# Kernel tuning notes

Hardware: AMD Instinct MI355X
Metric: run time of the kernel (lower is better)

Reference implementation:

```python
import jax, jax.numpy as jnp
import numpy as np

IN_OCT = 512
OUT_OCT = 512
BATCH = 512


def setup_inputs() -> dict:
    key = jax.random.key(0)
    kx, kw = jax.random.split(key)
    x = jax.random.normal(kx, (BATCH, IN_OCT * 8), dtype=jnp.float32)
    weight = jax.random.normal(kw, (OUT_OCT, IN_OCT, 8, 8), dtype=jnp.float32)
    bias = jnp.zeros((OUT_OCT, 8), dtype=jnp.float32)
    return {"x": x, "weight": weight, "bias": bias}


def reference(x, weight, bias):
    # x: [B, in_oct*8]; weight: [out_oct, in_oct, 8, 8]; bias: [out_oct, 8]
    B = x.shape[0]
    out_oct, in_oct = weight.shape[0], weight.shape[1]
    xo = x.reshape(B, in_oct, 8)
    # octonion_mul(x[:, j], weight[i, j]) applies the per-pair 8x8 octonion
    # left-multiplication matrix; summed over j it is one bilinear contraction.
    y = jnp.einsum("bjp,ijpk->bik", xo, weight) + bias[None, :, :]
    return y.reshape(B, out_oct * 8)
```

## Files before the change

kernel.cpp:

```cpp
#include <hip/hip_runtime.h>
#include <stdint.h>


#define M_DIM 512
#define N_DIM 4096
#define K_DIM 4096
#define KSPLIT 8
#define NIT ((K_DIM / KSPLIT) / 32)
#define PART_ELEMS (M_DIM * N_DIM)

typedef __bf16 bf16x8 __attribute__((ext_vector_type(8)));
typedef float f32x4 __attribute__((ext_vector_type(4)));

__device__ inline unsigned short f2bf(float f) {
  union { float f; unsigned int u; } v;
  v.f = f;
  unsigned int u = v.u;
  unsigned int r = (u + 0x7fffu + ((u >> 16) & 1u)) >> 16;
  return (unsigned short)r;
}

__global__ __launch_bounds__(256) void prep_kernel(
    const float* __restrict__ x, const float* __restrict__ w,
    const float* __restrict__ bias, unsigned short* __restrict__ abf,
    unsigned short* __restrict__ bt, float* __restrict__ out) {
  const int bid = blockIdx.x;
  const int t = threadIdx.x;
  if (bid < 4096) {
    __shared__ __align__(16) unsigned short lT[8][512];
    const int i = bid >> 3;
    const int jg = bid & 7;
    const float4* src =
        (const float4*)(w + (size_t)i * 32768 + jg * 4096 + t * 16);
    float4 v0 = src[0], v1 = src[1], v2 = src[2], v3 = src[3];
    const int jp = (t >> 2) * 8 + (t & 3) * 2;
    const float* lo = (const float*)&v0;
    const float* hi = (const float*)&v2;
#pragma unroll
    for (int k = 0; k < 4; ++k) {
      unsigned int pk =
          (unsigned int)f2bf(lo[k]) | ((unsigned int)f2bf(hi[k]) << 16);
      *(unsigned int*)&lT[k][jp] = pk;
    }
    lo = (const float*)&v1;
    hi = (const float*)&v3;
#pragma unroll
    for (int k = 0; k < 4; ++k) {
      unsigned int pk =
          (unsigned int)f2bf(lo[k]) | ((unsigned int)f2bf(hi[k]) << 16);
      *(unsigned int*)&lT[k + 4][jp] = pk;
    }
    __syncthreads();
    const int r = t >> 5, c = t & 31;
    const uint4* s = (const uint4*)&lT[r][c * 16];
    uint4* d = (uint4*)(bt + (size_t)(i * 8 + r) * K_DIM + jg * 512 + c * 16);
    d[0] = s[0];
    d[1] = s[1];
  } else if (bid < 5120) {
    int g = (bid - 4096) * 256 + t;
    const float4* xi = (const float4*)x;
    float4 a = xi[g * 2];
    float4 b = xi[g * 2 + 1];
    __attribute__((aligned(16))) unsigned short o[8] = {
        f2bf(a.x), f2bf(a.y), f2bf(a.z), f2bf(a.w),
        f2bf(b.x), f2bf(b.y), f2bf(b.z), f2bf(b.w)};
    *(uint4*)(abf + (size_t)g * 8) = *(const uint4*)o;
  } else {
    int g = (bid - 5120) * 256 + t;
    int el = g * 4;
    int col = el & (N_DIM - 1);
    *(float4*)(out + el) = *(const float4*)(bias + col);
  }
}

__device__ inline void gld16(const void* g, void* l) {
  __builtin_amdgcn_global_load_lds(
      (const __attribute__((address_space(1))) unsigned int*)g,
      (__attribute__((address_space(3))) unsigned int*)l, 16, 0, 0);
}

__global__ __launch_bounds__(512, 4) void gemm_kernel(
    const unsigned short* __restrict__ A, const unsigned short* __restrict__ Bt,
    float* __restrict__ out, float* __restrict__ part, int use_atomic) {
  __shared__ __align__(16) char lds[2][24 * 1024];
  const int t = threadIdx.x;
  const int n0 = blockIdx.x * 256;
  const int m0 = blockIdx.y * 128;
  const int z = blockIdx.z;
  const int kc0 = z * (K_DIM / KSPLIT);
  const int w = t >> 6;
  const int lane = t & 63;
  const int wr = w >> 2;
  const int wc = w & 3;
  const int lrow = lane & 15;
  const int kb = lane >> 4;

  f32x4 acc[4][4] = {};

  const size_t aOff = (size_t)(m0 + (t >> 2)) * K_DIM + kc0 + (t & 3) * 8;
  const size_t bOff0 = (size_t)(n0 + (t >> 2)) * K_DIM + kc0 + (t & 3) * 8;
  const size_t bOff1 = bOff0 + (size_t)128 * K_DIM;

  auto issue = [&](int it) {
    char* buf = lds[it & 1];
    gld16(A + aOff + it * 32, buf + t * 16);
    gld16(Bt + bOff0 + it * 32, buf + 8192 + t * 16);
    gld16(Bt + bOff1 + it * 32, buf + 16384 + t * 16);
  };

  issue(0);
  for (int it = 0; it < NIT; ++it) {
    __syncthreads();
    if (it + 1 < NIT) issue(it + 1);
    const unsigned short* cA = (const unsigned short*)lds[it & 1];
    const unsigned short* cB = cA + 4096;

    bf16x8 af[4], bfr[4];
#pragma unroll
    for (int mt = 0; mt < 4; ++mt)
      af[mt] = *(const bf16x8*)(cA + (wr * 64 + mt * 16 + lrow) * 32 + kb * 8);
#pragma unroll
    for (int nt = 0; nt < 4; ++nt)
      bfr[nt] = *(const bf16x8*)(cB + (wc * 64 + nt * 16 + lrow) * 32 + kb * 8);
#pragma unroll
    for (int mt = 0; mt < 4; ++mt)
#pragma unroll
      for (int nt = 0; nt < 4; ++nt)
        acc[mt][nt] = __builtin_amdgcn_mfma_f32_16x16x32_bf16(
            af[mt], bfr[nt], acc[mt][nt], 0, 0, 0);
  }

#pragma unroll
  for (int mt = 0; mt < 4; ++mt) {
    const int gmb = m0 + wr * 64 + mt * 16 + kb * 4;
#pragma unroll
    for (int nt = 0; nt < 4; ++nt) {
      const int gn = n0 + wc * 64 + nt * 16 + lrow;
      if (use_atomic) {
#pragma unroll
        for (int r = 0; r < 4; ++r)
          atomicAdd(out + (size_t)(gmb + r) * N_DIM + gn, acc[mt][nt][r]);
      } else {
        float* p = part + (size_t)z * PART_ELEMS;
#pragma unroll
        for (int r = 0; r < 4; ++r)
          p[(size_t)(gmb + r) * N_DIM + gn] = acc[mt][nt][r];
      }
    }
  }
}

__global__ __launch_bounds__(256) void reduce_kernel(
    const float* __restrict__ part, const float* __restrict__ bias,
    float* __restrict__ out) {
  const int g = blockIdx.x * 256 + threadIdx.x;
  const float4* p = (const float4*)part;
  const int Q = PART_ELEMS / 4;
  float4 r = ((const float4*)bias)[g & (N_DIM / 4 - 1)];
#pragma unroll
  for (int z = 0; z < KSPLIT; ++z) {
    float4 s = p[(size_t)g + (size_t)z * Q];
    r.x += s.x;
    r.y += s.y;
    r.z += s.z;
    r.w += s.w;
  }
  ((float4*)out)[g] = r;
}

extern "C" void kernel_launch(void* const* d_in, const int* in_sizes, int n_in,
                              void* d_out, int out_size, void* d_ws,
                              size_t ws_size, hipStream_t stream) {
  const float* x = (const float*)d_in[0];
  const float* w = (const float*)d_in[1];
  const float* bias = (const float*)d_in[2];
  float* out = (float*)d_out;

  unsigned short* abf = (unsigned short*)d_ws;
  unsigned short* bt = abf + (size_t)M_DIM * K_DIM;
  float* part = (float*)((char*)d_ws + 36u * 1024 * 1024);

  const bool have_ws = ws_size >= 101ull * 1024 * 1024;
  const int use_atomic = have_ws ? 0 : 1;

  prep_kernel<<<use_atomic ? 7168 : 5120, 256, 0, stream>>>(x, w, bias, abf,
                                                            bt, out);

  dim3 grid(N_DIM / 256, M_DIM / 128, KSPLIT);
  gemm_kernel<<<grid, 512, 0, stream>>>(abf, bt, out, part, use_atomic);

  if (!use_atomic)
    reduce_kernel<<<PART_ELEMS / 4 / 256, 256, 0, stream>>>(part, bias, out);
}
```

Before: 149.1 us.

## Fuse weight bf16 conversion and transpose into GEMM tile loading

Drops the separate weight conversion pass, which wrote a transposed bf16 copy of the 64 MB fp32 weight. The GEMM now reads fp32 weights directly, converts them in registers and writes them to LDS, prefetching one iteration ahead. Tiles become 512x64 with KSPLIT reduced to 4, which also shrinks the partial-sum buffer and the workspace requirement. The risk is uncoalesced strided fp32 weight loads, with only half the threads loading W, and lower occupancy from the larger LDS footprint.

```diff
diff --git a/kernel.cpp b/kernel.cpp
--- a/kernel.cpp
+++ b/kernel.cpp
@@ -5,8 +5,9 @@
 #define M_DIM 512
 #define N_DIM 4096
 #define K_DIM 4096
-#define KSPLIT 8
-#define NIT ((K_DIM / KSPLIT) / 32)
+#define KSPLIT 4
+#define KC (K_DIM / KSPLIT)
+#define NIT (KC / 32)
 #define PART_ELEMS (M_DIM * N_DIM)
 
 typedef __bf16 bf16x8 __attribute__((ext_vector_type(8)));
@@ -21,43 +22,12 @@
 }
 
 __global__ __launch_bounds__(256) void prep_kernel(
-    const float* __restrict__ x, const float* __restrict__ w,
-    const float* __restrict__ bias, unsigned short* __restrict__ abf,
-    unsigned short* __restrict__ bt, float* __restrict__ out) {
+    const float* __restrict__ x, const float* __restrict__ bias,
+    unsigned short* __restrict__ abf, float* __restrict__ out) {
   const int bid = blockIdx.x;
   const int t = threadIdx.x;
-  if (bid < 4096) {
-    __shared__ __align__(16) unsigned short lT[8][512];
-    const int i = bid >> 3;
-    const int jg = bid & 7;
-    const float4* src =
-        (const float4*)(w + (size_t)i * 32768 + jg * 4096 + t * 16);
-    float4 v0 = src[0], v1 = src[1], v2 = src[2], v3 = src[3];
-    const int jp = (t >> 2) * 8 + (t & 3) * 2;
-    const float* lo = (const float*)&v0;
-    const float* hi = (const float*)&v2;
-#pragma unroll
-    for (int k = 0; k < 4; ++k) {
-      unsigned int pk =
-          (unsigned int)f2bf(lo[k]) | ((unsigned int)f2bf(hi[k]) << 16);
-      *(unsigned int*)&lT[k][jp] = pk;
-    }
-    lo = (const float*)&v1;
-    hi = (const float*)&v3;
-#pragma unroll
-    for (int k = 0; k < 4; ++k) {
-      unsigned int pk =
-          (unsigned int)f2bf(lo[k]) | ((unsigned int)f2bf(hi[k]) << 16);
-      *(unsigned int*)&lT[k + 4][jp] = pk;
-    }
-    __syncthreads();
-    const int r = t >> 5, c = t & 31;
-    const uint4* s = (const uint4*)&lT[r][c * 16];
-    uint4* d = (uint4*)(bt + (size_t)(i * 8 + r) * K_DIM + jg * 512 + c * 16);
-    d[0] = s[0];
-    d[1] = s[1];
-  } else if (bid < 5120) {
-    int g = (bid - 4096) * 256 + t;
+  if (bid < 1024) {
+    int g = bid * 256 + t;
     const float4* xi = (const float4*)x;
     float4 a = xi[g * 2];
     float4 b = xi[g * 2 + 1];
@@ -66,7 +36,7 @@
         f2bf(b.x), f2bf(b.y), f2bf(b.z), f2bf(b.w)};
     *(uint4*)(abf + (size_t)g * 8) = *(const uint4*)o;
   } else {
-    int g = (bid - 5120) * 256 + t;
+    int g = (bid - 1024) * 256 + t;
     int el = g * 4;
     int col = el & (N_DIM - 1);
     *(float4*)(out + el) = *(const float4*)(bias + col);
@@ -79,63 +49,92 @@
       (__attribute__((address_space(3))) unsigned int*)l, 16, 0, 0);
 }
 
-__global__ __launch_bounds__(512, 4) void gemm_kernel(
-    const unsigned short* __restrict__ A, const unsigned short* __restrict__ Bt,
+__global__ __launch_bounds__(512, 2) void gemm_kernel(
+    const unsigned short* __restrict__ A, const float* __restrict__ W,
     float* __restrict__ out, float* __restrict__ part, int use_atomic) {
-  __shared__ __align__(16) char lds[2][24 * 1024];
+  __shared__ __align__(16) char lds[2][36 * 1024];
   const int t = threadIdx.x;
-  const int n0 = blockIdx.x * 256;
-  const int m0 = blockIdx.y * 128;
+  const int bn = blockIdx.x;
+  const int n0 = bn * 64;
   const int z = blockIdx.z;
-  const int kc0 = z * (K_DIM / KSPLIT);
+  const int kc0 = z * KC;
   const int w = t >> 6;
   const int lane = t & 63;
-  const int wr = w >> 2;
-  const int wc = w & 3;
   const int lrow = lane & 15;
   const int kb = lane >> 4;
 
   f32x4 acc[4][4] = {};
 
-  const size_t aOff = (size_t)(m0 + (t >> 2)) * K_DIM + kc0 + (t & 3) * 8;
-  const size_t bOff0 = (size_t)(n0 + (t >> 2)) * K_DIM + kc0 + (t & 3) * 8;
-  const size_t bOff1 = bOff0 + (size_t)128 * K_DIM;
-
-  auto issue = [&](int it) {
+  auto issueA = [&](int it) {
     char* buf = lds[it & 1];
-    gld16(A + aOff + it * 32, buf + t * 16);
-    gld16(Bt + bOff0 + it * 32, buf + 8192 + t * 16);
-    gld16(Bt + bOff1 + it * 32, buf + 16384 + t * 16);
+#pragma unroll
+    for (int q = 0; q < 4; ++q) {
+      const int seg = t + q * 512;
+      gld16(A + (size_t)(seg >> 2) * K_DIM + kc0 + it * 32 + (seg & 3) * 8,
+            buf + t * 16 + q * 8192);
+    }
   };
 
-  issue(0);
+  const int wi = t >> 5;
+  const int jl = (t >> 3) & 3;
+  const int wk = t & 7;
+  const float* wcol =
+      W + ((size_t)(bn * 8 + wi) * 512 + (size_t)(z * 128) + jl) * 64 + wk;
+
+  float wcur[8], wnxt[8];
+  auto loadW = [&](int it, float* r) {
+    if (t < 256) {
+      const float* p = wcol + (size_t)it * 4 * 64;
+#pragma unroll
+      for (int pp = 0; pp < 8; ++pp) r[pp] = p[pp * 8];
+    }
+  };
+  auto writeW = [&](int it, const float* r) {
+    if (t < 256) {
+      __attribute__((aligned(16))) unsigned short o[8];
+#pragma unroll
+      for (int pp = 0; pp < 8; ++pp) o[pp] = f2bf(r[pp]);
+      *(uint4*)(lds[it & 1] + 32768 + (wi * 8 + wk) * 64 + jl * 16) =
+          *(const uint4*)o;
+    }
+  };
+
+  issueA(0);
+  loadW(0, wcur);
+  writeW(0, wcur);
+
   for (int it = 0; it < NIT; ++it) {
     __syncthreads();
-    if (it + 1 < NIT) issue(it + 1);
+    if (it + 1 < NIT) {
+      issueA(it + 1);
+      loadW(it + 1, wnxt);
+    }
     const unsigned short* cA = (const unsigned short*)lds[it & 1];
-    const unsigned short* cB = cA + 4096;
+    const unsigned short* cB = (const unsigned short*)(lds[it & 1] + 32768);
 
     bf16x8 af[4], bfr[4];
 #pragma unroll
     for (int mt = 0; mt < 4; ++mt)
-      af[mt] = *(const bf16x8*)(cA + (wr * 64 + mt * 16 + lrow) * 32 + kb * 8);
+      af[mt] = *(const bf16x8*)(cA + (w * 64 + mt * 16 + lrow) * 32 + kb * 8);
 #pragma unroll
     for (int nt = 0; nt < 4; ++nt)
-      bfr[nt] = *(const bf16x8*)(cB + (wc * 64 + nt * 16 + lrow) * 32 + kb * 8);
+      bfr[nt] = *(const bf16x8*)(cB + (nt * 16 + lrow) * 32 + kb * 8);
 #pragma unroll
     for (int mt = 0; mt < 4; ++mt)
 #pragma unroll
       for (int nt = 0; nt < 4; ++nt)
         acc[mt][nt] = __builtin_amdgcn_mfma_f32_16x16x32_bf16(
             af[mt], bfr[nt], acc[mt][nt], 0, 0, 0);
+
+    if (it + 1 < NIT) writeW(it + 1, wnxt);
   }
 
 #pragma unroll
   for (int mt = 0; mt < 4; ++mt) {
-    const int gmb = m0 + wr * 64 + mt * 16 + kb * 4;
+    const int gmb = w * 64 + mt * 16 + kb * 4;
 #pragma unroll
     for (int nt = 0; nt < 4; ++nt) {
-      const int gn = n0 + wc * 64 + nt * 16 + lrow;
+      const int gn = n0 + nt * 16 + lrow;
       if (use_atomic) {
 #pragma unroll
         for (int r = 0; r < 4; ++r)
@@ -177,17 +176,15 @@
   float* out = (float*)d_out;
 
   unsigned short* abf = (unsigned short*)d_ws;
-  unsigned short* bt = abf + (size_t)M_DIM * K_DIM;
-  float* part = (float*)((char*)d_ws + 36u * 1024 * 1024);
+  float* part = (float*)((char*)d_ws + 4u * 1024 * 1024);
 
-  const bool have_ws = ws_size >= 101ull * 1024 * 1024;
+  const bool have_ws = ws_size >= 37ull * 1024 * 1024;
   const int use_atomic = have_ws ? 0 : 1;
 
-  prep_kernel<<<use_atomic ? 7168 : 5120, 256, 0, stream>>>(x, w, bias, abf,
-                                                            bt, out);
+  prep_kernel<<<use_atomic ? 3072 : 1024, 256, 0, stream>>>(x, bias, abf, out);
 
-  dim3 grid(N_DIM / 256, M_DIM / 128, KSPLIT);
-  gemm_kernel<<<grid, 512, 0, stream>>>(abf, bt, out, part, use_atomic);
+  dim3 grid(N_DIM / 64, 1, KSPLIT);
+  gemm_kernel<<<grid, 512, 0, stream>>>(abf, w, out, part, use_atomic);
 
   if (!use_atomic)
     reduce_kernel<<<PART_ELEMS / 4 / 256, 256, 0, stream>>>(part, bias, out);
```

Measured after the change: 142.9 us. 4.2% less time.
